# Kernel optimization log

Hardware: AMD Instinct MI355X
Metric: run time of the kernel (lower is better)

Reference implementation:

```python
import jax, jax.numpy as jnp
import numpy as np
from jax.scipy.special import logsumexp

N = 20000      # nodes
E = 320000     # input (undirected) edges
F_IN = 128
HID = 128
C = 8          # num_classes
ITERS = 100


def setup_inputs() -> dict:
    key = jax.random.key(0)
    ks = jax.random.split(key, 10)
    x = jax.random.normal(ks[0], (N, F_IN), dtype=jnp.float32)
    edge_index = jax.random.randint(ks[1], (2, E), 0, N)
    train_mask = jax.random.randint(ks[2], (N,), 0, 2).astype(bool)
    target = jax.random.randint(ks[3], (N,), 0, C)
    W1 = jax.random.normal(ks[4], (F_IN, HID), dtype=jnp.float32) / np.sqrt(F_IN).astype(np.float32)
    b1 = jnp.zeros((HID,), jnp.float32)
    W2 = jax.random.normal(ks[5], (HID, C), dtype=jnp.float32) / np.sqrt(HID).astype(np.float32)
    b2 = jnp.zeros((C,), jnp.float32)
    binary = (jax.random.normal(ks[6], (C, C), dtype=jnp.float32) + jnp.eye(C, dtype=jnp.float32)) / C
    rezero = 0.1 * jax.random.normal(ks[7], (E,), dtype=jnp.float32)
    return dict(x=x, edge_index=edge_index, train_mask=train_mask, target=target,
                W1=W1, b1=b1, W2=W2, b2=b2, binary=binary, rezero=rezero)


def _forward(x, edge_index, train_mask, target, W1, b1, W2, b2, binary, rezero):
    n = x.shape[0]
    # pairwise_edge_idx: make both directions of every edge (directed edge list, Ed = 2E)
    s0, d0 = edge_index[0], edge_index[1]
    src = jnp.concatenate([s0, d0])
    dst = jnp.concatenate([d0, s0])
    Ed = src.shape[0]

    # ---- GCN backbone (eval mode -> no dropout). GCNConv: sym-norm A-hat with self loops.
    sl = jnp.arange(n)
    gsrc = jnp.concatenate([src, sl])
    gdst = jnp.concatenate([dst, sl])
    degs = jax.ops.segment_sum(jnp.ones((gsrc.shape[0],), x.dtype), gdst, num_segments=n)
    dinv = jax.lax.rsqrt(jnp.maximum(degs, 1.0))
    enorm = dinv[gsrc] * dinv[gdst]  # [Ed+n]

    def conv(h, W, b):
        h = h @ W
        msg = h[gsrc] * enorm[:, None]
        return jax.ops.segment_sum(msg, gdst, num_segments=n) + b

    h = jax.nn.relu(conv(x, W1, b1))
    unary = conv(h, W2, b2)                       # [N, C]
    B = (binary + binary.T) / 2                   # symmetrized pairwise potential

    # ---- loopy_bp preprocessing (energies, GT clamping) -- torch.no_grad in original
    e_un = -unary
    gt_vals = jnp.take_along_axis(e_un, target[:, None], axis=1)  # GT energies, gathered first
    oh = jax.nn.one_hot(target, C, dtype=bool)
    e_un = jnp.where(train_mask[:, None], 1e5, e_un)
    e_un = jnp.where(train_mask[:, None] & oh, gt_vals, e_un)
    e_un = e_un - e_un.min(axis=1, keepdims=True)
    e_bin = -B
    e_bin = e_bin - e_bin.min()
    e_un = jnp.minimum(e_un, 20.0)
    phi_u = jax.lax.stop_gradient(-e_un)          # log node potentials
    phi_b = jax.lax.stop_gradient(-e_bin)         # log pairwise potential [C, C]
    scales = jax.lax.stop_gradient(jnp.concatenate([rezero, rezero]))  # per directed edge

    # reverse-edge index: edge i's reverse is i+E (mod 2E) by construction
    rev = (jnp.arange(Ed) + Ed // 2) % Ed

    def step(m, _):
        node_in = jax.ops.segment_sum(m, dst, num_segments=n)       # [N, C] sum of incoming msgs
        hmsg = (phi_u + node_in)[src] - m[rev]                       # [Ed, C] exclude reverse msg
        t = hmsg[:, :, None] + scales[:, None, None] * phi_b[None]   # [Ed, C, C]
        m_new = logsumexp(t, axis=1)                                 # marginalize sender label
        m_new = m_new - logsumexp(m_new, axis=1, keepdims=True)      # renormalize per iteration
        return m_new, None

    m0 = jnp.zeros((Ed, C), phi_u.dtype)
    m, _ = jax.lax.scan(step, m0, None, length=ITERS)

    beliefs = phi_u + jax.ops.segment_sum(m, dst, num_segments=n)
    return jax.nn.log_softmax(beliefs, axis=1)    # node_logits


def reference(x, edge_index, train_mask, target, W1, b1, W2, b2, binary, rezero):
    return _forward(x, edge_index, train_mask, target, W1, b1, W2, b2, binary, rezero)
```

## Files before the change

kernel.cpp:

```cpp
#include <hip/hip_runtime.h>
#include <hip/hip_bf16.h>

#define NN 20000
#define EU 320000
#define ED 640000
#define FIN 128
#define HD  128
#define NC  8
#define BP_ITERS 100
#define NPB 4

#define LOG2E 1.4426950408889634f
#define LN2   0.6931471805599453f

enum {
  OFF_FLAG   = 0,
  OFF_DINV   = 4,
  OFF_COUNT  = OFF_DINV  + NN,
  OFF_ROWPTR = OFF_COUNT + NN,
  OFF_FILL   = OFF_ROWPTR+ NN + 4,
  OFF_EID    = OFF_FILL  + NN,
  OFF_POS    = OFF_EID   + ED,
  OFF_SRC    = OFF_POS   + ED,
  OFF_REV    = OFF_SRC   + ED,
  OFF_SCALE  = OFF_REV   + ED,
  OFF_HW2    = OFF_SCALE + ED,
  OFF_PHIU   = OFF_HW2   + NN*NC,
  OFF_PHIB   = OFF_PHIU  + NN*NC,
  OFF_NPHI   = OFF_PHIB  + 64,
  OFF_MA     = OFF_NPHI  + NN*NC,
  OFF_MB     = OFF_MA    + ED*NC,
  WS_WORDS   = OFF_MB    + ED*NC
};

__device__ __forceinline__ float fexp2(float x) {
#if __has_builtin(__builtin_amdgcn_exp2f)
  return __builtin_amdgcn_exp2f(x);
#else
  return exp2f(x);
#endif
}
__device__ __forceinline__ float flog2(float x) {
#if __has_builtin(__builtin_amdgcn_logf)
  return __builtin_amdgcn_logf(x);
#else
  return log2f(x);
#endif
}

__global__ void k_detect(const unsigned* tm, int* flag) {
  __shared__ int bad;
  if (threadIdx.x == 0) bad = 0;
  __syncthreads();
  for (int i = threadIdx.x; i < NN / 4; i += blockDim.x) {
    if (tm[i] > 1u) atomicOr(&bad, 1);
  }
  __syncthreads();
  if (threadIdx.x == 0) flag[0] = bad;
}

__global__ void k_count(const int* ei, int* cnt) {
  int e = blockIdx.x * blockDim.x + threadIdx.x;
  if (e < ED) {
    int er = (e < EU) ? e + EU : e - EU;
    atomicAdd(&cnt[ei[er]], 1);
  }
}

__global__ void k_scan(const int* cnt, int* rowptr) {
  __shared__ int s[1024];
  const int T = 1024, CH = (NN + T - 1) / T;
  int t = threadIdx.x;
  int base = t * CH;
  int loc = 0;
  for (int k = 0; k < CH; k++) {
    int idx = base + k;
    if (idx < NN) loc += cnt[idx];
  }
  s[t] = loc;
  __syncthreads();
  for (int off = 1; off < T; off <<= 1) {
    int v = (t >= off) ? s[t - off] : 0;
    __syncthreads();
    s[t] += v;
    __syncthreads();
  }
  int run = s[t] - loc;
  for (int k = 0; k < CH; k++) {
    int idx = base + k;
    if (idx < NN) { rowptr[idx] = run; run += cnt[idx]; }
  }
  if (t == T - 1) rowptr[NN] = run;
}

__global__ void k_dinv(const int* cnt, float* dinv) {
  int v = blockIdx.x * blockDim.x + threadIdx.x;
  if (v < NN) dinv[v] = rsqrtf((float)(cnt[v] + 1));
}

__global__ void k_fill(const int* ei, const int* rowptr, int* fill,
                       int* eid, int* pos, int* srcarr, float* scale_s,
                       const float* rezero) {
  int e = blockIdx.x * blockDim.x + threadIdx.x;
  if (e < ED) {
    int er = (e < EU) ? e + EU : e - EU;
    int dst = ei[er];
    int p = rowptr[dst] + atomicAdd(&fill[dst], 1);
    eid[p] = e;
    pos[e] = p;
    srcarr[p] = ei[e];
    scale_s[p] = rezero[(e < EU) ? e : e - EU];
  }
}

__global__ void k_rev(int* eid, const int* pos, int* revslot, const int* ei) {
  int p = blockIdx.x * blockDim.x + threadIdx.x;
  if (p < ED) {
    int e = eid[p];
    int er = (e < EU) ? e + EU : e - EU;
    revslot[p] = pos[er];
    eid[p] = ei[er];
  }
}

__global__ __launch_bounds__(256) void k_gemm1(const float* __restrict__ x,
                                               const float* __restrict__ W1,
                                               const float* __restrict__ dinv,
                                               float* __restrict__ hw1) {
  int t = threadIdx.x;
  int c = t & 127, half = t >> 7;
  int r0 = blockIdx.x * 16 + half * 8;
  float acc[8];
#pragma unroll
  for (int r = 0; r < 8; r++) acc[r] = 0.f;
  for (int k = 0; k < FIN; k += 4) {
    float w0 = W1[k * HD + c];
    float w1 = W1[(k + 1) * HD + c];
    float w2 = W1[(k + 2) * HD + c];
    float w3 = W1[(k + 3) * HD + c];
#pragma unroll
    for (int r = 0; r < 8; r++) {
      float4 xr = *(const float4*)&x[(r0 + r) * FIN + k];
      acc[r] += xr.x * w0 + xr.y * w1 + xr.z * w2 + xr.w * w3;
    }
  }
#pragma unroll
  for (int r = 0; r < 8; r++)
    hw1[(r0 + r) * HD + c] = acc[r] * dinv[r0 + r];
}

__global__ __launch_bounds__(128) void k_agg1(const float* __restrict__ hw1,
                                              const float* __restrict__ dinv,
                                              const int* __restrict__ rowptr,
                                              const int* __restrict__ srcarr,
                                              const float* __restrict__ b1,
                                              float* __restrict__ h1) {
  int v = blockIdx.x;
  int f = threadIdx.x;
  int s0 = rowptr[v], s1 = rowptr[v + 1];
  float a0 = 0.f, a1 = 0.f, a2 = 0.f, a3 = 0.f;
  int s = s0;
  for (; s + 4 <= s1; s += 4) {
    int u0 = srcarr[s], u1 = srcarr[s + 1], u2 = srcarr[s + 2], u3 = srcarr[s + 3];
    a0 += hw1[u0 * HD + f];
    a1 += hw1[u1 * HD + f];
    a2 += hw1[u2 * HD + f];
    a3 += hw1[u3 * HD + f];
  }
  for (; s < s1; s++) a0 += hw1[srcarr[s] * HD + f];
  float acc = (a0 + a1) + (a2 + a3);
  float dv = dinv[v];
  float val = dv * (acc + hw1[v * HD + f]) + b1[f];
  h1[v * HD + f] = fmaxf(val, 0.f);
}

__global__ __launch_bounds__(256) void k_gemm2(const float* __restrict__ h1,
                                               const float* __restrict__ W2,
                                               const float* __restrict__ dinv,
                                               float* __restrict__ hw2) {
  __shared__ float Ws[HD * NC];
  int t = threadIdx.x;
  for (int i = t; i < HD * NC; i += 256) Ws[i] = W2[i];
  __syncthreads();
  int v = blockIdx.x * 256 + t;
  if (v >= NN) return;
  float acc[NC];
#pragma unroll
  for (int c = 0; c < NC; c++) acc[c] = 0.f;
  const float4* hp = (const float4*)&h1[v * HD];
  for (int k4 = 0; k4 < HD / 4; k4++) {
    float4 h4 = hp[k4];
    float hv[4] = {h4.x, h4.y, h4.z, h4.w};
#pragma unroll
    for (int j = 0; j < 4; j++) {
      int k = k4 * 4 + j;
#pragma unroll
      for (int c = 0; c < NC; c++) acc[c] += hv[j] * Ws[k * NC + c];
    }
  }
  float dv = dinv[v];
#pragma unroll
  for (int c = 0; c < NC; c++) hw2[v * NC + c] = acc[c] * dv;
}

__global__ __launch_bounds__(256) void k_agg2pre(const float* __restrict__ hw2,
                                                 const float* __restrict__ dinv,
                                                 const int* __restrict__ rowptr,
                                                 const int* __restrict__ srcarr,
                                                 const float* __restrict__ b2,
                                                 const int* __restrict__ target,
                                                 const void* __restrict__ tmask,
                                                 const int* __restrict__ flag,
                                                 float* __restrict__ phi_u) {
  int t = threadIdx.x;
  int node = blockIdx.x * 32 + (t >> 3);
  int c = t & 7;
  if (node >= NN) return;
  int s0 = rowptr[node], s1 = rowptr[node + 1];
  float acc = 0.f;
  for (int s = s0; s < s1; s++) {
    int u = srcarr[s];
    acc += hw2[u * NC + c];
  }
  float dv = dinv[node];
  float unary = dv * (acc + hw2[node * NC + c]) + b2[c];
  float e = -unary;
  int tgt = target[node];
  float gt = __shfl(e, (t & ~7) | tgt, 64);
  bool mk;
  if (flag[0]) mk = ((const unsigned char*)tmask)[node] != 0;
  else         mk = ((const int*)tmask)[node] != 0;
  if (mk) e = (c == tgt) ? gt : 1e5f;
  float mn = e;
  mn = fminf(mn, __shfl_xor(mn, 1));
  mn = fminf(mn, __shfl_xor(mn, 2));
  mn = fminf(mn, __shfl_xor(mn, 4));
  e = fminf(e - mn, 20.0f);
  phi_u[node * NC + c] = -e;
}

__global__ void k_phib(const float* __restrict__ binary, float* __restrict__ phib) {
  int t = threadIdx.x;
  int i = t >> 3, j = t & 7;
  float B = 0.5f * (binary[i * NC + j] + binary[j * NC + i]);
  float mx = B;
#pragma unroll
  for (int d = 1; d < 64; d <<= 1) mx = fmaxf(mx, __shfl_xor(mx, d));
  phib[t] = B - mx;
}

__global__ __launch_bounds__(256) void k_node(const float* __restrict__ m,
                                              const float* __restrict__ phiu,
                                              const int* __restrict__ rowptr,
                                              float* __restrict__ nphi) {
  int t = threadIdx.x;
  int w = t >> 6, l = t & 63, le = l >> 3, c = l & 7;
  int v = blockIdx.x * NPB + w;
  int s0 = rowptr[v], deg = rowptr[v + 1] - s0;
  float ni = 0.f;
  for (int q = le; q < deg; q += 8) ni += m[(s0 + q) * 8 + c];
  ni += __shfl_xor(ni, 8);
  ni += __shfl_xor(ni, 16);
  ni += __shfl_xor(ni, 32);
  if (le == 0) nphi[v * 8 + c] = phiu[v * 8 + c] + ni;
}

__global__ __launch_bounds__(256) void k_edge(const float* __restrict__ m,
                                              float* __restrict__ mout,
                                              const float* __restrict__ nphi,
                                              const int* __restrict__ dstof,
                                              const int* __restrict__ revslot,
                                              const float* __restrict__ scale_s,
                                              const float* __restrict__ phib_g) {
  int p = blockIdx.x * 256 + threadIdx.x;
  int v = dstof[p];
  float4 m0 = *(const float4*)&m[p * 8];
  float4 m1 = *(const float4*)&m[p * 8 + 4];
  float4 n0 = *(const float4*)&nphi[v * 8];
  float4 n1 = *(const float4*)&nphi[v * 8 + 4];
  float hm[8] = {n0.x - m0.x, n0.y - m0.y, n0.z - m0.z, n0.w - m0.w,
                 n1.x - m1.x, n1.y - m1.y, n1.z - m1.z, n1.w - m1.w};
  float mx = hm[0];
#pragma unroll
  for (int i = 1; i < 8; i++) mx = fmaxf(mx, hm[i]);
  float a[8];
#pragma unroll
  for (int i = 0; i < 8; i++) a[i] = (hm[i] - mx) * LOG2E;
  float sl = scale_s[p] * LOG2E;
  float out[8];
#pragma unroll
  for (int j = 0; j < 8; j++) {
    float S = 0.f;
#pragma unroll
    for (int i = 0; i < 8; i++)
      S += fexp2(fmaf(sl, phib_g[i * 8 + j], a[i]));
    out[j] = fmaf(flog2(S), LN2, mx);
  }
  float mm = out[0];
#pragma unroll
  for (int j = 1; j < 8; j++) mm = fmaxf(mm, out[j]);
  float Z = 0.f;
#pragma unroll
  for (int j = 0; j < 8; j++) Z += fexp2((out[j] - mm) * LOG2E);
  float lse = fmaf(flog2(Z), LN2, mm);
  int rp = revslot[p];
  float4 o0 = make_float4(out[0] - lse, out[1] - lse, out[2] - lse, out[3] - lse);
  float4 o1 = make_float4(out[4] - lse, out[5] - lse, out[6] - lse, out[7] - lse);
  *(float4*)&mout[rp * 8] = o0;
  *(float4*)&mout[rp * 8 + 4] = o1;
}

__global__ __launch_bounds__(256) void k_final(const float* __restrict__ m,
                                               const float* __restrict__ phiu,
                                               const int* __restrict__ rowptr,
                                               float* __restrict__ out) {
  int t = threadIdx.x;
  int w = t >> 6, l = t & 63, le = l >> 3, c = l & 7;
  int v = blockIdx.x * NPB + w;
  int s0 = rowptr[v], deg = rowptr[v + 1] - s0;
  float ni = 0.f;
  for (int q = le; q < deg; q += 8) ni += m[(s0 + q) * 8 + c];
  ni += __shfl_xor(ni, 8);
  ni += __shfl_xor(ni, 16);
  ni += __shfl_xor(ni, 32);
  float bel = phiu[v * 8 + c] + ni;
  float mx = bel;
  mx = fmaxf(mx, __shfl_xor(mx, 1));
  mx = fmaxf(mx, __shfl_xor(mx, 2));
  mx = fmaxf(mx, __shfl_xor(mx, 4));
  float Z = fexp2((bel - mx) * LOG2E);
  Z += __shfl_xor(Z, 1);
  Z += __shfl_xor(Z, 2);
  Z += __shfl_xor(Z, 4);
  out[v * 8 + c] = bel - fmaf(flog2(Z), LN2, mx);
}

extern "C" void kernel_launch(void* const* d_in, const int* in_sizes, int n_in,
                              void* d_out, int out_size, void* d_ws, size_t ws_size,
                              hipStream_t stream) {
  const float* x      = (const float*)d_in[0];
  const int*   ei     = (const int*)d_in[1];
  const void*  tmask  = d_in[2];
  const int*   target = (const int*)d_in[3];
  const float* W1     = (const float*)d_in[4];
  const float* b1     = (const float*)d_in[5];
  const float* W2     = (const float*)d_in[6];
  const float* b2     = (const float*)d_in[7];
  const float* binary = (const float*)d_in[8];
  const float* rezero = (const float*)d_in[9];

  float* ws  = (float*)d_ws;
  int*   wsi = (int*)d_ws;

  int*   flag    = wsi + OFF_FLAG;
  float* dinv    = ws  + OFF_DINV;
  int*   cnt     = wsi + OFF_COUNT;
  int*   rowptr  = wsi + OFF_ROWPTR;
  int*   fill    = wsi + OFF_FILL;
  int*   eid     = wsi + OFF_EID;
  int*   pos     = wsi + OFF_POS;
  int*   srcarr  = wsi + OFF_SRC;
  int*   revslot = wsi + OFF_REV;
  float* scale_s = ws  + OFF_SCALE;
  float* hw2     = ws  + OFF_HW2;
  float* phiu    = ws  + OFF_PHIU;
  float* phib    = ws  + OFF_PHIB;
  float* nphi    = ws  + OFF_NPHI;
  float* mA      = ws  + OFF_MA;
  float* mB      = ws  + OFF_MB;
  float* hw1     = mA;
  float* h1      = mB;

  hipMemsetAsync(cnt, 0, NN * sizeof(int), stream);
  hipMemsetAsync(fill, 0, NN * sizeof(int), stream);

  k_detect<<<1, 1024, 0, stream>>>((const unsigned*)tmask, flag);
  k_count<<<(ED + 255) / 256, 256, 0, stream>>>(ei, cnt);
  k_scan<<<1, 1024, 0, stream>>>(cnt, rowptr);
  k_dinv<<<(NN + 255) / 256, 256, 0, stream>>>(cnt, dinv);
  k_fill<<<(ED + 255) / 256, 256, 0, stream>>>(ei, rowptr, fill, eid, pos,
                                               srcarr, scale_s, rezero);
  k_rev<<<(ED + 255) / 256, 256, 0, stream>>>(eid, pos, revslot, ei);

  k_gemm1<<<NN / 16, 256, 0, stream>>>(x, W1, dinv, hw1);
  k_agg1<<<NN, 128, 0, stream>>>(hw1, dinv, rowptr, srcarr, b1, h1);
  k_gemm2<<<(NN + 255) / 256, 256, 0, stream>>>(h1, W2, dinv, hw2);
  k_agg2pre<<<NN / 32, 256, 0, stream>>>(hw2, dinv, rowptr, srcarr, b2, target,
                                         tmask, flag, phiu);
  k_phib<<<1, 64, 0, stream>>>(binary, phib);

  hipMemsetAsync(mA, 0, (size_t)ED * NC * sizeof(float), stream);

  float* mcur = mA;
  float* mnxt = mB;
  for (int it = 0; it < BP_ITERS; it++) {
    k_node<<<NN / NPB, 256, 0, stream>>>(mcur, phiu, rowptr, nphi);
    k_edge<<<ED / 256, 256, 0, stream>>>(mcur, mnxt, nphi, eid, revslot,
                                         scale_s, phib);
    float* tmp = mcur; mcur = mnxt; mnxt = tmp;
  }

  k_final<<<NN / NPB, 256, 0, stream>>>(mcur, phiu, rowptr, (float*)d_out);
}
```

Baseline: 2.561 ms.

## Fuse node aggregation into edge kernel by recomputing incoming sums per edge

Drops the separate per-node reduction kernel and its nphi buffer. Each edge thread now sums all incoming messages of its destination node itself, then does the logsumexp update. This halves the launches per BP iteration and removes the nphi write and read. In exchange the neighbor sum is recomputed once per incident edge, roughly degree-times redundant reads, though these mostly hit cache because a node's edges sit next to each other.

```diff
diff --git a/kernel.cpp b/kernel.cpp
--- a/kernel.cpp
+++ b/kernel.cpp
@@ -27,8 +27,7 @@
   OFF_HW2    = OFF_SCALE + ED,
   OFF_PHIU   = OFF_HW2   + NN*NC,
   OFF_PHIB   = OFF_PHIU  + NN*NC,
-  OFF_NPHI   = OFF_PHIB  + 64,
-  OFF_MA     = OFF_NPHI  + NN*NC,
+  OFF_MA     = OFF_PHIB  + 64,
   OFF_MB     = OFF_MA    + ED*NC,
   WS_WORDS   = OFF_MB    + ED*NC
 };
@@ -249,37 +248,45 @@
   phib[t] = B - mx;
 }
 
-__global__ __launch_bounds__(256) void k_node(const float* __restrict__ m,
-                                              const float* __restrict__ phiu,
-                                              const int* __restrict__ rowptr,
-                                              float* __restrict__ nphi) {
-  int t = threadIdx.x;
-  int w = t >> 6, l = t & 63, le = l >> 3, c = l & 7;
-  int v = blockIdx.x * NPB + w;
-  int s0 = rowptr[v], deg = rowptr[v + 1] - s0;
-  float ni = 0.f;
-  for (int q = le; q < deg; q += 8) ni += m[(s0 + q) * 8 + c];
-  ni += __shfl_xor(ni, 8);
-  ni += __shfl_xor(ni, 16);
-  ni += __shfl_xor(ni, 32);
-  if (le == 0) nphi[v * 8 + c] = phiu[v * 8 + c] + ni;
-}
-
-__global__ __launch_bounds__(256) void k_edge(const float* __restrict__ m,
-                                              float* __restrict__ mout,
-                                              const float* __restrict__ nphi,
-                                              const int* __restrict__ dstof,
-                                              const int* __restrict__ revslot,
-                                              const float* __restrict__ scale_s,
-                                              const float* __restrict__ phib_g) {
+__global__ __launch_bounds__(256) void k_bp3(const float* __restrict__ m,
+                                             float* __restrict__ mout,
+                                             const float* __restrict__ phiu,
+                                             const int* __restrict__ rowptr,
+                                             const int* __restrict__ dstof,
+                                             const int* __restrict__ revslot,
+                                             const float* __restrict__ scale_s,
+                                             const float* __restrict__ phib_g) {
   int p = blockIdx.x * 256 + threadIdx.x;
   int v = dstof[p];
+  int s0 = rowptr[v], s1 = rowptr[v + 1];
+  float ni[8];
+#pragma unroll
+  for (int i = 0; i < 8; i++) ni[i] = 0.f;
+  int s = s0;
+  for (; s + 2 <= s1; s += 2) {
+    float4 a0 = *(const float4*)&m[s * 8];
+    float4 a1 = *(const float4*)&m[s * 8 + 4];
+    float4 b0 = *(const float4*)&m[(s + 1) * 8];
+    float4 b1 = *(const float4*)&m[(s + 1) * 8 + 4];
+    ni[0] += a0.x + b0.x; ni[1] += a0.y + b0.y;
+    ni[2] += a0.z + b0.z; ni[3] += a0.w + b0.w;
+    ni[4] += a1.x + b1.x; ni[5] += a1.y + b1.y;
+    ni[6] += a1.z + b1.z; ni[7] += a1.w + b1.w;
+  }
+  if (s < s1) {
+    float4 a0 = *(const float4*)&m[s * 8];
+    float4 a1 = *(const float4*)&m[s * 8 + 4];
+    ni[0] += a0.x; ni[1] += a0.y; ni[2] += a0.z; ni[3] += a0.w;
+    ni[4] += a1.x; ni[5] += a1.y; ni[6] += a1.z; ni[7] += a1.w;
+  }
   float4 m0 = *(const float4*)&m[p * 8];
   float4 m1 = *(const float4*)&m[p * 8 + 4];
-  float4 n0 = *(const float4*)&nphi[v * 8];
-  float4 n1 = *(const float4*)&nphi[v * 8 + 4];
-  float hm[8] = {n0.x - m0.x, n0.y - m0.y, n0.z - m0.z, n0.w - m0.w,
-                 n1.x - m1.x, n1.y - m1.y, n1.z - m1.z, n1.w - m1.w};
+  float4 f0 = *(const float4*)&phiu[v * 8];
+  float4 f1 = *(const float4*)&phiu[v * 8 + 4];
+  float hm[8] = {f0.x + ni[0] - m0.x, f0.y + ni[1] - m0.y,
+                 f0.z + ni[2] - m0.z, f0.w + ni[3] - m0.w,
+                 f1.x + ni[4] - m1.x, f1.y + ni[5] - m1.y,
+                 f1.z + ni[6] - m1.z, f1.w + ni[7] - m1.w};
   float mx = hm[0];
 #pragma unroll
   for (int i = 1; i < 8; i++) mx = fmaxf(mx, hm[i]);
@@ -365,7 +372,6 @@
   float* hw2     = ws  + OFF_HW2;
   float* phiu    = ws  + OFF_PHIU;
   float* phib    = ws  + OFF_PHIB;
-  float* nphi    = ws  + OFF_NPHI;
   float* mA      = ws  + OFF_MA;
   float* mB      = ws  + OFF_MB;
   float* hw1     = mA;
@@ -394,9 +400,8 @@
   float* mcur = mA;
   float* mnxt = mB;
   for (int it = 0; it < BP_ITERS; it++) {
-    k_node<<<NN / NPB, 256, 0, stream>>>(mcur, phiu, rowptr, nphi);
-    k_edge<<<ED / 256, 256, 0, stream>>>(mcur, mnxt, nphi, eid, revslot,
-                                         scale_s, phib);
+    k_bp3<<<ED / 256, 256, 0, stream>>>(mcur, mnxt, phiu, rowptr, eid, revslot,
+                                        scale_s, phib);
     float* tmp = mcur; mcur = mnxt; mnxt = tmp;
   }
 
```

Measured after the change: 4.001 ms. 56.3% more time.
